# Kernel optimization log

Measured on AMD Instinct MI355X. Metric: run time of the kernel, lower is better.

The kernel has to match this reference:

```python
import jax, jax.numpy as jnp
import numpy as np

N = 50000          # num nodes
E = 800000         # num edges (before self loops)
DIM_IN = 128
HID = 32           # per-head hidden of conv1
HEADS = 8          # heads of conv1
DIM_OUT = 16       # output classes (conv2, 1 head, concat=False)
NEG_SLOPE = 0.2    # GATConv default leaky_relu slope


def gat_conv(x, W, a_src, a_dst, bias, src, dst, heads, out_ch, concat):
    """PyG GATConv (self-loops already appended to src/dst).
    x: [N, F_in], W: [F_in, heads*out_ch], a_src/a_dst: [heads, out_ch], bias matches output.
    """
    n = x.shape[0]
    h = (x @ W).reshape(n, heads, out_ch)                    # [N, H, C]
    al_src = jnp.einsum('nhc,hc->nh', h, a_src)              # [N, H]
    al_dst = jnp.einsum('nhc,hc->nh', h, a_dst)              # [N, H]
    e = jax.nn.leaky_relu(al_src[src] + al_dst[dst], NEG_SLOPE)   # [E', H]
    # segment softmax over edges grouped by target node (dst)
    emax = jax.ops.segment_max(e, dst, num_segments=n)       # [N, H]
    ee = jnp.exp(e - emax[dst])                              # [E', H]
    denom = jax.ops.segment_sum(ee, dst, num_segments=n)     # [N, H]
    alpha = ee / (denom[dst] + 1e-16)                        # [E', H]
    msg = h[src] * alpha[:, :, None]                         # [E', H, C]
    out = jax.ops.segment_sum(msg, dst, num_segments=n)      # [N, H, C]
    out = out.reshape(n, heads * out_ch) if concat else out.mean(axis=1)
    return out + bias


def setup_inputs() -> dict:
    key = jax.random.key(0)
    ks = jax.random.split(key, 12)
    x = jax.random.normal(ks[0], (N, DIM_IN), dtype=jnp.float32)
    edge_index = jax.random.randint(ks[1], (2, E), 0, N, dtype=jnp.int64)
    s = 0.1
    W1 = jax.random.normal(ks[2], (DIM_IN, HEADS * HID), dtype=jnp.float32) * s
    a1_src = jax.random.normal(ks[3], (HEADS, HID), dtype=jnp.float32) * s
    a1_dst = jax.random.normal(ks[4], (HEADS, HID), dtype=jnp.float32) * s
    b1 = jnp.zeros((HEADS * HID,), dtype=jnp.float32)
    W2 = jax.random.normal(ks[5], (HEADS * HID, DIM_OUT), dtype=jnp.float32) * s
    a2_src = jax.random.normal(ks[6], (1, DIM_OUT), dtype=jnp.float32) * s
    a2_dst = jax.random.normal(ks[7], (1, DIM_OUT), dtype=jnp.float32) * s
    b2 = jnp.zeros((DIM_OUT,), dtype=jnp.float32)
    return {"x": x, "edge_index": edge_index, "W1": W1, "a1_src": a1_src,
            "a1_dst": a1_dst, "b1": b1, "W2": W2, "a2_src": a2_src,
            "a2_dst": a2_dst, "b2": b2}


def reference(x, edge_index, W1, a1_src, a1_dst, b1, W2, a2_src, a2_dst, b2):
    # add self loops (GATConv default add_self_loops=True)
    loops = jnp.arange(N, dtype=edge_index.dtype)
    src = jnp.concatenate([edge_index[0], loops])
    dst = jnp.concatenate([edge_index[1], loops])
    # dropout layers are identity in eval mode
    h = gat_conv(x, W1, a1_src, a1_dst, b1, src, dst, HEADS, HID, concat=True)
    h = jax.nn.elu(h)
    out = gat_conv(h, W2, a2_src, a2_dst, b2, src, dst, 1, DIM_OUT, concat=False)
    return jax.nn.log_softmax(out, axis=1)
```

## Files before the change

kernel.cpp:

```cpp
#include <hip/hip_runtime.h>
#include <hip/hip_bf16.h>

#define NN 50000
#define EE 800000
#define EP (EE + NN)
#define DIN 128
#define HID 32
#define HEADS 8
#define C1 (HEADS * HID)
#define DOUT 16
#define NW1 3125
#define SH 9
#define NB 98
#define CAP 16384
#define EPT 8
#define BBLK (256 * EPT)

typedef __attribute__((ext_vector_type(8))) short short8;
typedef __attribute__((ext_vector_type(4))) float float4v;
typedef __attribute__((ext_vector_type(2))) float float2v;

__device__ inline unsigned short f2bf(float f) {
    __hip_bfloat16 b = __float2bfloat16(f);
    return *reinterpret_cast<unsigned short*>(&b);
}
__device__ inline float bflo(unsigned u) {
    union { unsigned int i; float f; } x;
    x.i = u << 16;
    return x.f;
}
__device__ inline float bfhi(unsigned u) {
    union { unsigned int i; float f; } x;
    x.i = u & 0xffff0000u;
    return x.f;
}
__device__ inline float bf2f(unsigned short u) {
    union { unsigned int i; float f; } x;
    x.i = ((unsigned int)u) << 16;
    return x.f;
}

__global__ void k_prepfw(const float* __restrict__ W1, const float* __restrict__ a1s,
                         const float* __restrict__ a1d, const float* __restrict__ W2,
                         unsigned short* __restrict__ w1frag,
                         unsigned short* __restrict__ w2frag,
                         int* __restrict__ cntb) {
    int i = blockIdx.x * 256 + threadIdx.x;
    if (blockIdx.x == 0 && threadIdx.x < NB) cntb[threadIdx.x] = 0;
    if (i < 17 * 2048) {
        int j = i & 7, lane = (i >> 3) & 63, s = (i >> 9) & 3, c = i >> 11;
        int q = lane >> 4, m = lane & 15;
        int k = s * 32 + q * 8 + j;
        float val;
        if (c < 16) {
            val = W1[k * C1 + c * 16 + m];
        } else {
            int h = m & 7;
            const float* av = (m < 8) ? a1s : a1d;
            float acc = 0.f;
            #pragma unroll
            for (int j2 = 0; j2 < 32; j2++)
                acc += W1[k * C1 + h * 32 + j2] * av[h * 32 + j2];
            val = acc;
        }
        w1frag[i] = f2bf(val);
    } else if (i < 17 * 2048 + 8 * 512) {
        int j2 = i - 17 * 2048;
        int jj = j2 & 7, lane = (j2 >> 3) & 63, s = j2 >> 9;
        int q = lane >> 4, m = lane & 15;
        w2frag[j2] = f2bf(W2[(s * 32 + q * 8 + jj) * DOUT + m]);
    }
}

__global__ __launch_bounds__(256) void k_bucketA(const int* __restrict__ ei,
                                                 int* __restrict__ cntb,
                                                 unsigned* __restrict__ ebuf) {
    __shared__ int hist[4][NB];
    __shared__ int base[4][NB];
    int t = threadIdx.x;
    int wave = t >> 6;
    for (int i = t; i < 4 * NB; i += 256) ((int*)hist)[i] = 0;
    __syncthreads();
    int e0 = blockIdx.x * BBLK;
    int s[EPT], d[EPT], r[EPT];
    #pragma unroll
    for (int j = 0; j < EPT; j++) {
        int e = e0 + j * 256 + t;
        int ss = 0, dd = -1;
        if (e < EE) { ss = ei[e]; dd = ei[EE + e]; }
        else if (e < EP) { ss = e - EE; dd = ss; }
        s[j] = ss; d[j] = dd;
        if (dd >= 0) r[j] = atomicAdd(&hist[wave][dd >> SH], 1);
    }
    __syncthreads();
    if (t < NB) {
        int h0 = hist[0][t], h1 = hist[1][t], h2 = hist[2][t], h3 = hist[3][t];
        int tot = h0 + h1 + h2 + h3;
        int bb = tot ? atomicAdd(&cntb[t], tot) : 0;
        base[0][t] = bb;
        base[1][t] = bb + h0;
        base[2][t] = bb + h0 + h1;
        base[3][t] = bb + h0 + h1 + h2;
    }
    __syncthreads();
    #pragma unroll
    for (int j = 0; j < EPT; j++) {
        if (d[j] >= 0) {
            int b = d[j] >> SH;
            ebuf[b * CAP + base[wave][b] + r[j]] =
                ((unsigned)s[j] << SH) | (unsigned)(d[j] & 511);
        }
    }
}

__global__ __launch_bounds__(1024) void k_csr(const int* __restrict__ cntb,
                                              const unsigned* __restrict__ ebuf,
                                              int* __restrict__ row_ptr,
                                              int* __restrict__ esrc) {
    __shared__ int sdeg[512];
    __shared__ int wtot[8];
    __shared__ int bpart[2];
    int b = blockIdx.x;
    int t = threadIdx.x;
    int lane = t & 63, wave = t >> 6;
    int nodes0 = b << SH;
    if (t < 512) sdeg[t] = 0;
    if (t < 128) {
        int v = (t < b) ? cntb[t] : 0;
        #pragma unroll
        for (int off = 1; off < 64; off <<= 1) v += __shfl_xor(v, off, 64);
        if (lane == 0) bpart[wave] = v;
    }
    __syncthreads();
    int baseS = bpart[0] + bpart[1];
    int cnt = cntb[b];
    const unsigned* eb = ebuf + b * CAP;
    for (int i = t; i < cnt; i += 1024)
        atomicAdd(&sdeg[eb[i] & 511], 1);
    __syncthreads();
    int v = (t < 512) ? sdeg[t] : 0;
    int inc = v;
    #pragma unroll
    for (int off = 1; off < 64; off <<= 1) {
        int u = __shfl_up(inc, off, 64);
        if (lane >= off) inc += u;
    }
    if (t < 512 && lane == 63) wtot[wave] = inc;
    __syncthreads();
    if (wave == 0 && lane < 8) {
        int w = wtot[lane];
        int iw = w;
        #pragma unroll
        for (int off = 1; off < 8; off <<= 1) {
            int u = __shfl_up(iw, off, 64);
            if (lane >= off) iw += u;
        }
        wtot[lane] = iw - w;
    }
    __syncthreads();
    int excl = inc - v + ((t < 512) ? wtot[wave] : 0);
    __syncthreads();
    if (t < 512) {
        sdeg[t] = excl;
        int node = nodes0 + t;
        if (node < NN) row_ptr[node] = baseS + excl;
    }
    __syncthreads();
    for (int i = t; i < cnt; i += 1024) {
        unsigned e = eb[i];
        int pos = atomicAdd(&sdeg[e & 511], 1);
        esrc[baseS + pos] = (int)(e >> SH);
    }
    if (b == 0 && t == 0) row_ptr[NN] = EP;
}

__global__ __launch_bounds__(256) void k_gemm1(const float* __restrict__ x,
                                               const unsigned short* __restrict__ w1frag,
                                               unsigned char* __restrict__ h1f8,
                                               float* __restrict__ al1sd,
                                               unsigned short* __restrict__ al1s8) {
    int wid = (blockIdx.x * 256 + threadIdx.x) >> 6;
    int lane = threadIdx.x & 63;
    if (wid >= NW1) return;
    int nb = wid * 16;
    int m = lane & 15, quad = lane >> 4;
    const float* xrow = x + (nb + m) * DIN;

    float4 xf[8];
    #pragma unroll
    for (int s = 0; s < 4; s++) {
        xf[2 * s]     = *(const float4*)(xrow + s * 32 + quad * 8);
        xf[2 * s + 1] = *(const float4*)(xrow + s * 32 + quad * 8 + 4);
    }
    short8 bfr[4];
    #pragma unroll
    for (int s = 0; s < 4; s++) {
        unsigned short* bp = (unsigned short*)&bfr[s];
        float4 f0 = xf[2 * s], f1 = xf[2 * s + 1];
        bp[0] = f2bf(f0.x); bp[1] = f2bf(f0.y); bp[2] = f2bf(f0.z); bp[3] = f2bf(f0.w);
        bp[4] = f2bf(f1.x); bp[5] = f2bf(f1.y); bp[6] = f2bf(f1.z); bp[7] = f2bf(f1.w);
    }

    float4v acc[17];
    #pragma unroll
    for (int c = 0; c < 17; c++) acc[c] = (float4v){0.f, 0.f, 0.f, 0.f};

    #pragma unroll
    for (int s = 0; s < 4; s++) {
        const unsigned short* fp = w1frag + (s * 64 + lane) * 8;
        #pragma unroll
        for (int c = 0; c < 17; c++) {
            short8 afrag = *(const short8*)(fp + c * 2048);
            acc[c] = __builtin_amdgcn_mfma_f32_16x16x32_bf16(afrag, bfr[s], acc[c], 0, 0, 0);
        }
    }

    int node = nb + m;
    #pragma unroll
    for (int c = 0; c < 16; c++) {
        unsigned pk = 0;
        pk = __builtin_amdgcn_cvt_pk_fp8_f32(acc[c][0], acc[c][1], pk, false);
        pk = __builtin_amdgcn_cvt_pk_fp8_f32(acc[c][2], acc[c][3], pk, true);
        *(unsigned*)(h1f8 + node * C1 + c * 16 + quad * 4) = pk;
    }
    *(float4*)(al1sd + node * 16 + quad * 4) =
        make_float4(acc[16][0], acc[16][1], acc[16][2], acc[16][3]);
    if (quad < 2) {
        uint2 pk;
        pk.x = (unsigned)f2bf(acc[16][0]) | ((unsigned)f2bf(acc[16][1]) << 16);
        pk.y = (unsigned)f2bf(acc[16][2]) | ((unsigned)f2bf(acc[16][3]) << 16);
        *(uint2*)(al1s8 + node * 8 + quad * 4) = pk;
    }
}

__global__ __launch_bounds__(256) void k_agg1(const int* __restrict__ row_ptr,
                                              const int* __restrict__ esrc,
                                              const unsigned char* __restrict__ h1f8,
                                              const unsigned short* __restrict__ al1s8,
                                              const float* __restrict__ al1sd,
                                              const float* __restrict__ b1,
                                              unsigned short* __restrict__ helu_b) {
    __shared__ float wbuf[4][64 * 8];
    __shared__ int   sbuf[4][64];
    int wslot = threadIdx.x >> 6;
    int L = threadIdx.x & 63;
    int d = (blockIdx.x * 256 + threadIdx.x) >> 6;
    int h = L >> 3;
    int start = row_ptr[d], end = row_ptr[d + 1];
    float4 ald0 = *(const float4*)(al1sd + d * 16 + 8);
    float4 ald1 = *(const float4*)(al1sd + d * 16 + 12);
    float* wrow = wbuf[wslot];
    int* srow = sbuf[wslot];
    float denom = 0.f;
    float4 acc = make_float4(0.f, 0.f, 0.f, 0.f);
    const int Lofs = L * 4;

    for (int base = start; base < end; base += 64) {
        int cnt = min(64, end - base);
        int s = d;
        float wv0 = 0.f, wv1 = 0.f, wv2 = 0.f, wv3 = 0.f;
        float wv4 = 0.f, wv5 = 0.f, wv6 = 0.f, wv7 = 0.f;
        if (L < cnt) {
            s = esrc[base + L];
            uint4 as = *(const uint4*)(al1s8 + s * 8);
            float e;
            e = bflo(as.x) + ald0.x; e = e > 0.f ? e : 0.2f * e; wv0 = __expf(e);
            e = bfhi(as.x) + ald0.y; e = e > 0.f ? e : 0.2f * e; wv1 = __expf(e);
            e = bflo(as.y) + ald0.z; e = e > 0.f ? e : 0.2f * e; wv2 = __expf(e);
            e = bfhi(as.y) + ald0.w; e = e > 0.f ? e : 0.2f * e; wv3 = __expf(e);
            e = bflo(as.z) + ald1.x; e = e > 0.f ? e : 0.2f * e; wv4 = __expf(e);
            e = bfhi(as.z) + ald1.y; e = e > 0.f ? e : 0.2f * e; wv5 = __expf(e);
            e = bflo(as.w) + ald1.z; e = e > 0.f ? e : 0.2f * e; wv6 = __expf(e);
            e = bfhi(as.w) + ald1.w; e = e > 0.f ? e : 0.2f * e; wv7 = __expf(e);
        }
        srow[L] = s;
        *(float4*)&wrow[L * 8]     = make_float4(wv0, wv1, wv2, wv3);
        *(float4*)&wrow[L * 8 + 4] = make_float4(wv4, wv5, wv6, wv7);
        int cnt4 = (cnt + 3) & ~3;
        for (int i = 0; i < cnt4; i += 4) {
            int s0 = srow[i], s1 = srow[i + 1], s2 = srow[i + 2], s3 = srow[i + 3];
            float x0 = wrow[i * 8 + h];
            float x1 = wrow[i * 8 + 8 + h];
            float x2 = wrow[i * 8 + 16 + h];
            float x3 = wrow[i * 8 + 24 + h];
            unsigned v0 = *(const unsigned*)(h1f8 + s0 * C1 + Lofs);
            unsigned v1 = *(const unsigned*)(h1f8 + s1 * C1 + Lofs);
            unsigned v2 = *(const unsigned*)(h1f8 + s2 * C1 + Lofs);
            unsigned v3 = *(const unsigned*)(h1f8 + s3 * C1 + Lofs);
            denom += (x0 + x1) + (x2 + x3);
            float2v a, b;
            a = __builtin_amdgcn_cvt_pk_f32_fp8(v0, false);
            b = __builtin_amdgcn_cvt_pk_f32_fp8(v0, true);
            acc.x += x0 * a.x; acc.y += x0 * a.y; acc.z += x0 * b.x; acc.w += x0 * b.y;
            a = __builtin_amdgcn_cvt_pk_f32_fp8(v1, false);
            b = __builtin_amdgcn_cvt_pk_f32_fp8(v1, true);
            acc.x += x1 * a.x; acc.y += x1 * a.y; acc.z += x1 * b.x; acc.w += x1 * b.y;
            a = __builtin_amdgcn_cvt_pk_f32_fp8(v2, false);
            b = __builtin_amdgcn_cvt_pk_f32_fp8(v2, true);
            acc.x += x2 * a.x; acc.y += x2 * a.y; acc.z += x2 * b.x; acc.w += x2 * b.y;
            a = __builtin_amdgcn_cvt_pk_f32_fp8(v3, false);
            b = __builtin_amdgcn_cvt_pk_f32_fp8(v3, true);
            acc.x += x3 * a.x; acc.y += x3 * a.y; acc.z += x3 * b.x; acc.w += x3 * b.y;
        }
    }
    float inv = 1.0f / (denom + 1e-16f);
    float4 bv = *(const float4*)(b1 + Lofs);
    float o0 = acc.x * inv + bv.x;
    float o1 = acc.y * inv + bv.y;
    float o2 = acc.z * inv + bv.z;
    float o3 = acc.w * inv + bv.w;
    o0 = o0 > 0.f ? o0 : __expf(o0) - 1.0f;
    o1 = o1 > 0.f ? o1 : __expf(o1) - 1.0f;
    o2 = o2 > 0.f ? o2 : __expf(o2) - 1.0f;
    o3 = o3 > 0.f ? o3 : __expf(o3) - 1.0f;
    uint2 pk;
    pk.x = (unsigned)f2bf(o0) | ((unsigned)f2bf(o1) << 16);
    pk.y = (unsigned)f2bf(o2) | ((unsigned)f2bf(o3) << 16);
    *(uint2*)(helu_b + d * C1 + Lofs) = pk;
}

__global__ __launch_bounds__(256) void k_gemm2(const unsigned short* __restrict__ helu_b,
                                               const unsigned short* __restrict__ w2frag,
                                               const float* __restrict__ a2s,
                                               const float* __restrict__ a2d,
                                               unsigned short* __restrict__ h2b,
                                               float* __restrict__ al2s,
                                               float* __restrict__ al2d) {
    int wid = (blockIdx.x * 256 + threadIdx.x) >> 6;
    int lane = threadIdx.x & 63;
    int nb = wid * 16;
    if (nb >= NN) return;
    int m = lane & 15, quad = lane >> 4;

    const unsigned short* wp2 = w2frag + lane * 8;
    float4v acc = {0.f, 0.f, 0.f, 0.f};
    const unsigned short* arow = helu_b + (nb + m) * C1 + quad * 8;
    #pragma unroll
    for (int s = 0; s < 8; s++) {
        short8 afrag = *(const short8*)(arow + s * 32);
        short8 bfrag = *(const short8*)(wp2 + s * 512);
        acc = __builtin_amdgcn_mfma_f32_16x16x32_bf16(afrag, bfrag, acc, 0, 0, 0);
    }

    float as_c = a2s[m], ad_c = a2d[m];
    #pragma unroll
    for (int r = 0; r < 4; r++) {
        int node = nb + quad * 4 + r;
        float val = acc[r];
        h2b[node * DOUT + m] = f2bf(val);
        float ps = val * as_c;
        float pd = val * ad_c;
        ps += __shfl_xor(ps, 1, 64); ps += __shfl_xor(ps, 2, 64);
        ps += __shfl_xor(ps, 4, 64); ps += __shfl_xor(ps, 8, 64);
        pd += __shfl_xor(pd, 1, 64); pd += __shfl_xor(pd, 2, 64);
        pd += __shfl_xor(pd, 4, 64); pd += __shfl_xor(pd, 8, 64);
        if (m == 0) {
            al2s[node] = ps;
            al2d[node] = pd;
        }
    }
}

__global__ __launch_bounds__(256) void k_agg2(const int* __restrict__ row_ptr,
                                              const int* __restrict__ esrc,
                                              const unsigned short* __restrict__ h2b,
                                              const float* __restrict__ al2s,
                                              const float* __restrict__ al2d,
                                              const float* __restrict__ b2,
                                              float* __restrict__ out) {
    __shared__ float wbuf2[4][64];
    __shared__ int   sbuf2[4][64];
    int wslot = threadIdx.x >> 6;
    int L = threadIdx.x & 63;
    int n = (blockIdx.x * 256 + threadIdx.x) >> 6;
    if (n >= NN) return;
    int p = L & 7, g = L >> 3;
    int start = row_ptr[n], end = row_ptr[n + 1];
    float ald = al2d[n];
    float* wrow = wbuf2[wslot];
    int* srow = sbuf2[wslot];
    float acc0 = 0.f, acc1 = 0.f, denom = 0.f;

    for (int base = start; base < end; base += 64) {
        int cnt = min(64, end - base);
        int s = n; float w = 0.f;
        if (L < cnt) {
            s = esrc[base + L];
            float e = al2s[s] + ald;
            e = e > 0.f ? e : 0.2f * e;
            w = __expf(e);
        }
        srow[L] = s;
        wrow[L] = w;
        int cnt8 = (cnt + 7) & ~7;
        for (int i = 0; i < cnt8; i += 8) {
            int idx = i + g;
            int ss = srow[idx];
            float ww = wrow[idx];
            unsigned v = *(const unsigned*)(h2b + ss * DOUT + p * 2);
            acc0 += ww * bflo(v);
            acc1 += ww * bfhi(v);
            denom += ww;
        }
    }
    acc0 += __shfl_xor(acc0, 8, 64);  acc0 += __shfl_xor(acc0, 16, 64);  acc0 += __shfl_xor(acc0, 32, 64);
    acc1 += __shfl_xor(acc1, 8, 64);  acc1 += __shfl_xor(acc1, 16, 64);  acc1 += __shfl_xor(acc1, 32, 64);
    denom += __shfl_xor(denom, 8, 64); denom += __shfl_xor(denom, 16, 64); denom += __shfl_xor(denom, 32, 64);
    float inv = 1.0f / (denom + 1e-16f);
    float2 bv = *(const float2*)(b2 + p * 2);
    float val0 = acc0 * inv + bv.x;
    float val1 = acc1 * inv + bv.y;
    float m = fmaxf(val0, val1);
    #pragma unroll
    for (int mm = 1; mm < 8; mm <<= 1) m = fmaxf(m, __shfl_xor(m, mm, 64));
    float se = __expf(val0 - m) + __expf(val1 - m);
    #pragma unroll
    for (int mm = 1; mm < 8; mm <<= 1) se += __shfl_xor(se, mm, 64);
    float lse = m + __logf(se);
    if (L < 8) {
        float2 o = make_float2(val0 - lse, val1 - lse);
        *(float2*)(out + n * DOUT + p * 2) = o;
    }
}

extern "C" void kernel_launch(void* const* d_in, const int* in_sizes, int n_in,
                              void* d_out, int out_size, void* d_ws, size_t ws_size,
                              hipStream_t stream) {
    const float* x   = (const float*)d_in[0];
    const int*   ei  = (const int*)d_in[1];
    const float* W1  = (const float*)d_in[2];
    const float* a1s = (const float*)d_in[3];
    const float* a1d = (const float*)d_in[4];
    const float* b1  = (const float*)d_in[5];
    const float* W2  = (const float*)d_in[6];
    const float* a2s = (const float*)d_in[7];
    const float* a2d = (const float*)d_in[8];
    const float* b2  = (const float*)d_in[9];
    float* outp = (float*)d_out;

    unsigned char* h1f8    = (unsigned char*)d_ws;
    unsigned short* helu_b = (unsigned short*)(h1f8 + NN * C1);
    unsigned short* h2b    = helu_b + NN * C1;
    unsigned short* w2frag = h2b + NN * DOUT;
    unsigned short* w1frag = w2frag + 8 * 512;
    unsigned short* al1s8  = w1frag + 17 * 2048;
    float* al1sd = (float*)(al1s8 + NN * 8);
    float* al2sb = al1sd + NN * 16;
    float* al2db = al2sb + NN;
    int* row_ptr = (int*)(al2db + NN);
    int* esrc    = row_ptr + NN + 1;
    int* cntb    = esrc + EP;
    unsigned* ebuf = (unsigned*)helu_b;

    k_prepfw<<<(17 * 2048 + 8 * 512 + 255) / 256, 256, 0, stream>>>(W1, a1s, a1d, W2, w1frag, w2frag, cntb);
    k_bucketA<<<(EP + BBLK - 1) / BBLK, 256, 0, stream>>>(ei, cntb, ebuf);
    k_gemm1<<<(NW1 * 64 + 255) / 256, 256, 0, stream>>>(x, w1frag, h1f8, al1sd, al1s8);
    k_csr<<<NB, 1024, 0, stream>>>(cntb, ebuf, row_ptr, esrc);
    k_agg1<<<12500, 256, 0, stream>>>(row_ptr, esrc, h1f8, al1s8, al1sd, b1, helu_b);
    k_gemm2<<<(NW1 * 64 + 255) / 256, 256, 0, stream>>>(helu_b, w2frag, a2s, a2d, h2b, al2sb, al2db);
    k_agg2<<<(NN * 64 + 255) / 256, 256, 0, stream>>>(row_ptr, esrc, h2b, al2sb, al2db, b2, outp);
}
```

Measured before the change: 205.3 us.

## Merge GEMM1 and edge bucketing launches, halve bucket width, unroll aggregation by eight

GEMM1 and the edge-bucketing kernel become one launch whose block index picks the role, so the two independent stages can run concurrently and one launch is saved. Buckets now cover 256 nodes instead of 512, which doubles the number of CSR blocks and raises parallelism in the CSR build, at the cost of more global atomics on the bucket counters. The layer-1 aggregation loop issues eight gathers before consuming them, to give more memory-level parallelism. Risks are bucket overflow if a 256-node bucket gets more than 8192 edges, and higher register pressure in the fused kernel.

```diff
diff --git a/kernel.cpp b/kernel.cpp
--- a/kernel.cpp
+++ b/kernel.cpp
@@ -10,11 +10,13 @@
 #define C1 (HEADS * HID)
 #define DOUT 16
 #define NW1 3125
-#define SH 9
-#define NB 98
-#define CAP 16384
+#define SH 8
+#define NB 196
+#define CAP 8192
 #define EPT 8
 #define BBLK (256 * EPT)
+#define GB ((NW1 * 64 + 255) / 256)
+#define BB ((EP + BBLK - 1) / BBLK)
 
 typedef __attribute__((ext_vector_type(8))) short short8;
 typedef __attribute__((ext_vector_type(4))) float float4v;
@@ -72,43 +74,104 @@
     }
 }
 
-__global__ __launch_bounds__(256) void k_bucketA(const int* __restrict__ ei,
-                                                 int* __restrict__ cntb,
-                                                 unsigned* __restrict__ ebuf) {
+__global__ __launch_bounds__(256) void k_g1bkt(const float* __restrict__ x,
+                                               const unsigned short* __restrict__ w1frag,
+                                               unsigned char* __restrict__ h1f8,
+                                               float* __restrict__ al1sd,
+                                               unsigned short* __restrict__ al1s8,
+                                               const int* __restrict__ ei,
+                                               int* __restrict__ cntb,
+                                               unsigned* __restrict__ ebuf) {
     __shared__ int hist[4][NB];
     __shared__ int base[4][NB];
-    int t = threadIdx.x;
-    int wave = t >> 6;
-    for (int i = t; i < 4 * NB; i += 256) ((int*)hist)[i] = 0;
-    __syncthreads();
-    int e0 = blockIdx.x * BBLK;
-    int s[EPT], d[EPT], r[EPT];
-    #pragma unroll
-    for (int j = 0; j < EPT; j++) {
-        int e = e0 + j * 256 + t;
-        int ss = 0, dd = -1;
-        if (e < EE) { ss = ei[e]; dd = ei[EE + e]; }
-        else if (e < EP) { ss = e - EE; dd = ss; }
-        s[j] = ss; d[j] = dd;
-        if (dd >= 0) r[j] = atomicAdd(&hist[wave][dd >> SH], 1);
-    }
-    __syncthreads();
-    if (t < NB) {
-        int h0 = hist[0][t], h1 = hist[1][t], h2 = hist[2][t], h3 = hist[3][t];
-        int tot = h0 + h1 + h2 + h3;
-        int bb = tot ? atomicAdd(&cntb[t], tot) : 0;
-        base[0][t] = bb;
-        base[1][t] = bb + h0;
-        base[2][t] = bb + h0 + h1;
-        base[3][t] = bb + h0 + h1 + h2;
-    }
-    __syncthreads();
-    #pragma unroll
-    for (int j = 0; j < EPT; j++) {
-        if (d[j] >= 0) {
-            int b = d[j] >> SH;
-            ebuf[b * CAP + base[wave][b] + r[j]] =
-                ((unsigned)s[j] << SH) | (unsigned)(d[j] & 511);
+    int bid = blockIdx.x;
+    if (bid < GB) {
+        int wid = (bid * 256 + threadIdx.x) >> 6;
+        int lane = threadIdx.x & 63;
+        if (wid >= NW1) return;
+        int nb = wid * 16;
+        int m = lane & 15, quad = lane >> 4;
+        const float* xrow = x + (nb + m) * DIN;
+
+        float4 xf[8];
+        #pragma unroll
+        for (int s = 0; s < 4; s++) {
+            xf[2 * s]     = *(const float4*)(xrow + s * 32 + quad * 8);
+            xf[2 * s + 1] = *(const float4*)(xrow + s * 32 + quad * 8 + 4);
+        }
+        short8 bfr[4];
+        #pragma unroll
+        for (int s = 0; s < 4; s++) {
+            unsigned short* bp = (unsigned short*)&bfr[s];
+            float4 f0 = xf[2 * s], f1 = xf[2 * s + 1];
+            bp[0] = f2bf(f0.x); bp[1] = f2bf(f0.y); bp[2] = f2bf(f0.z); bp[3] = f2bf(f0.w);
+            bp[4] = f2bf(f1.x); bp[5] = f2bf(f1.y); bp[6] = f2bf(f1.z); bp[7] = f2bf(f1.w);
+        }
+
+        float4v acc[17];
+        #pragma unroll
+        for (int c = 0; c < 17; c++) acc[c] = (float4v){0.f, 0.f, 0.f, 0.f};
+
+        #pragma unroll
+        for (int s = 0; s < 4; s++) {
+            const unsigned short* fp = w1frag + (s * 64 + lane) * 8;
+            #pragma unroll
+            for (int c = 0; c < 17; c++) {
+                short8 afrag = *(const short8*)(fp + c * 2048);
+                acc[c] = __builtin_amdgcn_mfma_f32_16x16x32_bf16(afrag, bfr[s], acc[c], 0, 0, 0);
+            }
+        }
+
+        int node = nb + m;
+        #pragma unroll
+        for (int c = 0; c < 16; c++) {
+            unsigned pk = 0;
+            pk = __builtin_amdgcn_cvt_pk_fp8_f32(acc[c][0], acc[c][1], pk, false);
+            pk = __builtin_amdgcn_cvt_pk_fp8_f32(acc[c][2], acc[c][3], pk, true);
+            *(unsigned*)(h1f8 + node * C1 + c * 16 + quad * 4) = pk;
+        }
+        *(float4*)(al1sd + node * 16 + quad * 4) =
+            make_float4(acc[16][0], acc[16][1], acc[16][2], acc[16][3]);
+        if (quad < 2) {
+            uint2 pk;
+            pk.x = (unsigned)f2bf(acc[16][0]) | ((unsigned)f2bf(acc[16][1]) << 16);
+            pk.y = (unsigned)f2bf(acc[16][2]) | ((unsigned)f2bf(acc[16][3]) << 16);
+            *(uint2*)(al1s8 + node * 8 + quad * 4) = pk;
+        }
+    } else {
+        int t = threadIdx.x;
+        int wave = t >> 6;
+        for (int i = t; i < 4 * NB; i += 256) ((int*)hist)[i] = 0;
+        __syncthreads();
+        int e0 = (bid - GB) * BBLK;
+        int s[EPT], d[EPT], r[EPT];
+        #pragma unroll
+        for (int j = 0; j < EPT; j++) {
+            int e = e0 + j * 256 + t;
+            int ss = 0, dd = -1;
+            if (e < EE) { ss = ei[e]; dd = ei[EE + e]; }
+            else if (e < EP) { ss = e - EE; dd = ss; }
+            s[j] = ss; d[j] = dd;
+            if (dd >= 0) r[j] = atomicAdd(&hist[wave][dd >> SH], 1);
+        }
+        __syncthreads();
+        if (t < NB) {
+            int h0 = hist[0][t], h1 = hist[1][t], h2 = hist[2][t], h3 = hist[3][t];
+            int tot = h0 + h1 + h2 + h3;
+            int bb = tot ? atomicAdd(&cntb[t], tot) : 0;
+            base[0][t] = bb;
+            base[1][t] = bb + h0;
+            base[2][t] = bb + h0 + h1;
+            base[3][t] = bb + h0 + h1 + h2;
+        }
+        __syncthreads();
+        #pragma unroll
+        for (int j = 0; j < EPT; j++) {
+            if (d[j] >= 0) {
+                int b = d[j] >> SH;
+                ebuf[b * CAP + base[wave][b] + r[j]] =
+                    ((unsigned)s[j] << SH) | (unsigned)(d[j] & 255);
+            }
         }
     }
 }
@@ -117,50 +180,50 @@
                                               const unsigned* __restrict__ ebuf,
                                               int* __restrict__ row_ptr,
                                               int* __restrict__ esrc) {
-    __shared__ int sdeg[512];
-    __shared__ int wtot[8];
-    __shared__ int bpart[2];
+    __shared__ int sdeg[256];
+    __shared__ int wtot[4];
+    __shared__ int bpart[4];
     int b = blockIdx.x;
     int t = threadIdx.x;
     int lane = t & 63, wave = t >> 6;
     int nodes0 = b << SH;
-    if (t < 512) sdeg[t] = 0;
-    if (t < 128) {
+    if (t < 256) sdeg[t] = 0;
+    if (t < 256) {
         int v = (t < b) ? cntb[t] : 0;
         #pragma unroll
         for (int off = 1; off < 64; off <<= 1) v += __shfl_xor(v, off, 64);
         if (lane == 0) bpart[wave] = v;
     }
     __syncthreads();
-    int baseS = bpart[0] + bpart[1];
+    int baseS = bpart[0] + bpart[1] + bpart[2] + bpart[3];
     int cnt = cntb[b];
     const unsigned* eb = ebuf + b * CAP;
     for (int i = t; i < cnt; i += 1024)
-        atomicAdd(&sdeg[eb[i] & 511], 1);
-    __syncthreads();
-    int v = (t < 512) ? sdeg[t] : 0;
+        atomicAdd(&sdeg[eb[i] & 255], 1);
+    __syncthreads();
+    int v = (t < 256) ? sdeg[t] : 0;
     int inc = v;
     #pragma unroll
     for (int off = 1; off < 64; off <<= 1) {
         int u = __shfl_up(inc, off, 64);
         if (lane >= off) inc += u;
     }
-    if (t < 512 && lane == 63) wtot[wave] = inc;
-    __syncthreads();
-    if (wave == 0 && lane < 8) {
+    if (t < 256 && lane == 63) wtot[wave] = inc;
+    __syncthreads();
+    if (wave == 0 && lane < 4) {
         int w = wtot[lane];
         int iw = w;
         #pragma unroll
-        for (int off = 1; off < 8; off <<= 1) {
+        for (int off = 1; off < 4; off <<= 1) {
             int u = __shfl_up(iw, off, 64);
             if (lane >= off) iw += u;
         }
         wtot[lane] = iw - w;
     }
     __syncthreads();
-    int excl = inc - v + ((t < 512) ? wtot[wave] : 0);
-    __syncthreads();
-    if (t < 512) {
+    int excl = inc - v + ((t < 256) ? wtot[wave] : 0);
+    __syncthreads();
+    if (t < 256) {
         sdeg[t] = excl;
         int node = nodes0 + t;
         if (node < NN) row_ptr[node] = baseS + excl;
@@ -168,69 +231,10 @@
     __syncthreads();
     for (int i = t; i < cnt; i += 1024) {
         unsigned e = eb[i];
-        int pos = atomicAdd(&sdeg[e & 511], 1);
+        int pos = atomicAdd(&sdeg[e & 255], 1);
         esrc[baseS + pos] = (int)(e >> SH);
     }
     if (b == 0 && t == 0) row_ptr[NN] = EP;
-}
-
-__global__ __launch_bounds__(256) void k_gemm1(const float* __restrict__ x,
-                                               const unsigned short* __restrict__ w1frag,
-                                               unsigned char* __restrict__ h1f8,
-                                               float* __restrict__ al1sd,
-                                               unsigned short* __restrict__ al1s8) {
-    int wid = (blockIdx.x * 256 + threadIdx.x) >> 6;
-    int lane = threadIdx.x & 63;
-    if (wid >= NW1) return;
-    int nb = wid * 16;
-    int m = lane & 15, quad = lane >> 4;
-    const float* xrow = x + (nb + m) * DIN;
-
-    float4 xf[8];
-    #pragma unroll
-    for (int s = 0; s < 4; s++) {
-        xf[2 * s]     = *(const float4*)(xrow + s * 32 + quad * 8);
-        xf[2 * s + 1] = *(const float4*)(xrow + s * 32 + quad * 8 + 4);
-    }
-    short8 bfr[4];
-    #pragma unroll
-    for (int s = 0; s < 4; s++) {
-        unsigned short* bp = (unsigned short*)&bfr[s];
-        float4 f0 = xf[2 * s], f1 = xf[2 * s + 1];
-        bp[0] = f2bf(f0.x); bp[1] = f2bf(f0.y); bp[2] = f2bf(f0.z); bp[3] = f2bf(f0.w);
-        bp[4] = f2bf(f1.x); bp[5] = f2bf(f1.y); bp[6] = f2bf(f1.z); bp[7] = f2bf(f1.w);
-    }
-
-    float4v acc[17];
-    #pragma unroll
-    for (int c = 0; c < 17; c++) acc[c] = (float4v){0.f, 0.f, 0.f, 0.f};
-
-    #pragma unroll
-    for (int s = 0; s < 4; s++) {
-        const unsigned short* fp = w1frag + (s * 64 + lane) * 8;
-        #pragma unroll
-        for (int c = 0; c < 17; c++) {
-            short8 afrag = *(const short8*)(fp + c * 2048);
-            acc[c] = __builtin_amdgcn_mfma_f32_16x16x32_bf16(afrag, bfr[s], acc[c], 0, 0, 0);
-        }
-    }
-
-    int node = nb + m;
-    #pragma unroll
-    for (int c = 0; c < 16; c++) {
-        unsigned pk = 0;
-        pk = __builtin_amdgcn_cvt_pk_fp8_f32(acc[c][0], acc[c][1], pk, false);
-        pk = __builtin_amdgcn_cvt_pk_fp8_f32(acc[c][2], acc[c][3], pk, true);
-        *(unsigned*)(h1f8 + node * C1 + c * 16 + quad * 4) = pk;
-    }
-    *(float4*)(al1sd + node * 16 + quad * 4) =
-        make_float4(acc[16][0], acc[16][1], acc[16][2], acc[16][3]);
-    if (quad < 2) {
-        uint2 pk;
-        pk.x = (unsigned)f2bf(acc[16][0]) | ((unsigned)f2bf(acc[16][1]) << 16);
-        pk.y = (unsigned)f2bf(acc[16][2]) | ((unsigned)f2bf(acc[16][3]) << 16);
-        *(uint2*)(al1s8 + node * 8 + quad * 4) = pk;
-    }
 }
 
 __global__ __launch_bounds__(256) void k_agg1(const int* __restrict__ row_ptr,
@@ -276,31 +280,24 @@
         srow[L] = s;
         *(float4*)&wrow[L * 8]     = make_float4(wv0, wv1, wv2, wv3);
         *(float4*)&wrow[L * 8 + 4] = make_float4(wv4, wv5, wv6, wv7);
-        int cnt4 = (cnt + 3) & ~3;
-        for (int i = 0; i < cnt4; i += 4) {
-            int s0 = srow[i], s1 = srow[i + 1], s2 = srow[i + 2], s3 = srow[i + 3];
-            float x0 = wrow[i * 8 + h];
-            float x1 = wrow[i * 8 + 8 + h];
-            float x2 = wrow[i * 8 + 16 + h];
-            float x3 = wrow[i * 8 + 24 + h];
-            unsigned v0 = *(const unsigned*)(h1f8 + s0 * C1 + Lofs);
-            unsigned v1 = *(const unsigned*)(h1f8 + s1 * C1 + Lofs);
-            unsigned v2 = *(const unsigned*)(h1f8 + s2 * C1 + Lofs);
-            unsigned v3 = *(const unsigned*)(h1f8 + s3 * C1 + Lofs);
-            denom += (x0 + x1) + (x2 + x3);
-            float2v a, b;
-            a = __builtin_amdgcn_cvt_pk_f32_fp8(v0, false);
-            b = __builtin_amdgcn_cvt_pk_f32_fp8(v0, true);
-            acc.x += x0 * a.x; acc.y += x0 * a.y; acc.z += x0 * b.x; acc.w += x0 * b.y;
-            a = __builtin_amdgcn_cvt_pk_f32_fp8(v1, false);
-            b = __builtin_amdgcn_cvt_pk_f32_fp8(v1, true);
-            acc.x += x1 * a.x; acc.y += x1 * a.y; acc.z += x1 * b.x; acc.w += x1 * b.y;
-            a = __builtin_amdgcn_cvt_pk_f32_fp8(v2, false);
-            b = __builtin_amdgcn_cvt_pk_f32_fp8(v2, true);
-            acc.x += x2 * a.x; acc.y += x2 * a.y; acc.z += x2 * b.x; acc.w += x2 * b.y;
-            a = __builtin_amdgcn_cvt_pk_f32_fp8(v3, false);
-            b = __builtin_amdgcn_cvt_pk_f32_fp8(v3, true);
-            acc.x += x3 * a.x; acc.y += x3 * a.y; acc.z += x3 * b.x; acc.w += x3 * b.y;
+        int cnt8 = (cnt + 7) & ~7;
+        for (int i = 0; i < cnt8; i += 8) {
+            unsigned v[8];
+            float xw[8];
+            #pragma unroll
+            for (int j = 0; j < 8; j++) {
+                int sj = srow[i + j];
+                xw[j] = wrow[(i + j) * 8 + h];
+                v[j] = *(const unsigned*)(h1f8 + sj * C1 + Lofs);
+            }
+            #pragma unroll
+            for (int j = 0; j < 8; j++) {
+                float2v a = __builtin_amdgcn_cvt_pk_f32_fp8(v[j], false);
+                float2v b = __builtin_amdgcn_cvt_pk_f32_fp8(v[j], true);
+                float xj = xw[j];
+                denom += xj;
+                acc.x += xj * a.x; acc.y += xj * a.y; acc.z += xj * b.x; acc.w += xj * b.y;
+            }
         }
     }
     float inv = 1.0f / (denom + 1e-16f);
@@ -453,8 +450,7 @@
     unsigned* ebuf = (unsigned*)helu_b;
 
     k_prepfw<<<(17 * 2048 + 8 * 512 + 255) / 256, 256, 0, stream>>>(W1, a1s, a1d, W2, w1frag, w2frag, cntb);
-    k_bucketA<<<(EP + BBLK - 1) / BBLK, 256, 0, stream>>>(ei, cntb, ebuf);
-    k_gemm1<<<(NW1 * 64 + 255) / 256, 256, 0, stream>>>(x, w1frag, h1f8, al1sd, al1s8);
+    k_g1bkt<<<GB + BB, 256, 0, stream>>>(x, w1frag, h1f8, al1sd, al1s8, ei, cntb, ebuf);
     k_csr<<<NB, 1024, 0, stream>>>(cntb, ebuf, row_ptr, esrc);
     k_agg1<<<12500, 256, 0, stream>>>(row_ptr, esrc, h1f8, al1s8, al1sd, b1, helu_b);
     k_gemm2<<<(NW1 * 64 + 255) / 256, 256, 0, stream>>>(helu_b, w2frag, a2s, a2d, h2b, al2sb, al2db);
```

Measured after the change: 200.8 us. 2.2% less time.
